# Kernel tuning notes

Hardware: AMD Instinct MI355X
Metric: run time of the kernel (lower is better)

## Reference

```python
import jax, jax.numpy as jnp
import numpy as np

N, E, F_IN, HID, NUM_CLASSES = 10000, 160000, 512, 1024, 100
NEG_SLOPE = 0.2  # PyG GATv2Conv default negative_slope


def setup_inputs() -> dict:
    key = jax.random.key(0)
    ks = jax.random.split(key, 10)
    return {
        "x": jax.random.normal(ks[0], (N, F_IN), jnp.float32),
        "edge_index": jax.random.randint(ks[1], (2, E), 0, N, dtype=jnp.int64)
        if jax.config.jax_enable_x64 else jax.random.randint(ks[1], (2, E), 0, N, dtype=jnp.int32),
        # GATv2Conv params (single head, out=1024): lin_l (source), lin_r (target), attention vector a, output bias
        "Wl": jax.random.normal(ks[2], (F_IN, HID), jnp.float32) / np.sqrt(F_IN),
        "bl": jnp.zeros((HID,), jnp.float32),
        "Wr": jax.random.normal(ks[3], (F_IN, HID), jnp.float32) / np.sqrt(F_IN),
        "br": jnp.zeros((HID,), jnp.float32),
        "att": jax.random.normal(ks[4], (HID,), jnp.float32) / np.sqrt(HID),
        "conv_b": jnp.zeros((HID,), jnp.float32),
        # MLP head: 1024 -> 512 -> 128 -> num_classes
        "W1": jax.random.normal(ks[5], (HID, 512), jnp.float32) / np.sqrt(HID),
        "b1": jnp.zeros((512,), jnp.float32),
        "W2": jax.random.normal(ks[6], (512, 128), jnp.float32) / np.sqrt(512),
        "b2": jnp.zeros((128,), jnp.float32),
        "Wc": jax.random.normal(ks[7], (128, NUM_CLASSES), jnp.float32) / np.sqrt(128),
        "bc": jnp.zeros((NUM_CLASSES,), jnp.float32),
    }


def _gatv2_conv(x, edge_index, Wl, bl, Wr, br, att, conv_b):
    """GATv2Conv, heads=1, add_self_loops=True, share_weights=False."""
    n = x.shape[0]
    loops = jnp.arange(n, dtype=edge_index.dtype)
    src = jnp.concatenate([edge_index[0], loops])  # message sources j
    dst = jnp.concatenate([edge_index[1], loops])  # message targets i
    xl = x @ Wl + bl  # [N, HID] source transform
    xr = x @ Wr + br  # [N, HID] target transform
    # e_ij = a^T LeakyReLU(xl_j + xr_i), per edge
    e = jax.nn.leaky_relu(xl[src] + xr[dst], negative_slope=NEG_SLOPE) @ att  # [E+N]
    # segment softmax over incoming edges of each target node (self-loops guarantee non-empty segments)
    m = jax.ops.segment_max(e, dst, num_segments=n)
    w = jnp.exp(e - m[dst])
    s = jax.ops.segment_sum(w, dst, num_segments=n)
    alpha = w / s[dst]  # [E+N]
    out = jax.ops.segment_sum(alpha[:, None] * xl[src], dst, num_segments=n)  # [N, HID]
    return out + conv_b


def reference(x, edge_index, Wl, bl, Wr, br, att, conv_b, W1, b1, W2, b2, Wc, bc):
    h = jax.nn.relu(_gatv2_conv(x, edge_index, Wl, bl, Wr, br, att, conv_b))
    h = jax.nn.relu(h @ W1 + b1)
    h = jax.nn.relu(h @ W2 + b2)
    return h @ Wc + bc
```

## Files before the change

kernel.cpp:

```cpp
#include <hip/hip_runtime.h>
#include <hip/hip_bf16.h>

constexpr int N_NODES = 10000;
constexpr int E_EDGES = 160000;
constexpr int F_IN    = 512;
constexpr int HID     = 1024;
constexpr int NCLS    = 100;
constexpr float NEG_SLOPE = 0.2f;

constexpr int BN = 128, BK = 32;
constexpr int M_PAD = 10112;
constexpr int DEG_CAP = 64;

typedef __attribute__((ext_vector_type(8))) short bf16x8;
typedef __attribute__((ext_vector_type(4))) float f32x4;
typedef __attribute__((ext_vector_type(2))) float f32x2;

__device__ inline void load_lds_16(const void* g, void* l) {
    __builtin_amdgcn_global_load_lds(
        (const __attribute__((address_space(1))) void*)g,
        (__attribute__((address_space(3))) void*)l, 16, 0, 0);
}

__device__ inline float rfl(float x) {
    return __builtin_bit_cast(float,
        __builtin_amdgcn_readfirstlane(__builtin_bit_cast(int, x)));
}

__device__ inline f32x2 bfpair(int d) {
    f32x2 r;
    r.x = __builtin_bit_cast(float, d << 16);
    r.y = __builtin_bit_cast(float, d & (int)0xffff0000);
    return r;
}

__device__ inline short4 cvt4(const f32x4 v, const float4 b, int relu) {
    float r0 = v[0] + b.x, r1 = v[1] + b.y, r2 = v[2] + b.z, r3 = v[3] + b.w;
    if (relu) {
        r0 = fmaxf(r0, 0.f); r1 = fmaxf(r1, 0.f);
        r2 = fmaxf(r2, 0.f); r3 = fmaxf(r3, 0.f);
    }
    short4 o;
    o.x = __builtin_bit_cast(short, __float2bfloat16(r0));
    o.y = __builtin_bit_cast(short, __float2bfloat16(r1));
    o.z = __builtin_bit_cast(short, __float2bfloat16(r2));
    o.w = __builtin_bit_cast(short, __float2bfloat16(r3));
    return o;
}

__global__ __launch_bounds__(256, 4) void gemm_mfma_64(
    const __hip_bfloat16* __restrict__ A, const __hip_bfloat16* __restrict__ Bt,
    const float* __restrict__ bias, int M, int K, int relu, int n_valid,
    __hip_bfloat16* __restrict__ Cb, int ldb)
{
    __shared__ __align__(16) short As[2][64 * BK];
    __shared__ __align__(16) short Bs[2][BN * BK];

    const int tid  = threadIdx.x;
    const int lane = tid & 63;
    const int w    = tid >> 6;
    const int m0   = blockIdx.y * 64;
    const int n0   = blockIdx.x * BN;

    f32x4 acc[4][2] = {};

    const int ca = tid;
    const int ra = ca >> 2, cca = (ca & 3) ^ ((ra >> 2) & 3);
    const int c0 = tid, c1 = tid + 256;
    const int r0 = c0 >> 2, cc0 = (c0 & 3) ^ ((r0 >> 2) & 3);
    const int r1 = c1 >> 2, cc1 = (c1 & 3) ^ ((r1 >> 2) & 3);

    const short* Ag  = (const short*)A + (size_t)(m0 + ra) * K + cca * 8;
    const short* Bg0 = (const short*)Bt + (size_t)(n0 + r0) * K + cc0 * 8;
    const short* Bg1 = (const short*)Bt + (size_t)(n0 + r1) * K + cc1 * 8;

    const int wn = w * 32;
    const int q  = lane >> 4;
    const int mr = lane & 15;
    const int sl = (q ^ (mr >> 2)) * 8;

    load_lds_16(Ag,  As[0] + ca * 8);
    load_lds_16(Bg0, Bs[0] + c0 * 8);
    load_lds_16(Bg1, Bs[0] + c1 * 8);

    int cur = 0;
    for (int k0 = 0; k0 < K; k0 += BK) {
        __syncthreads();
        const int nxt = cur ^ 1;
        const int kn = k0 + BK;
        if (kn < K) {
            load_lds_16(Ag + kn,  As[nxt] + ca * 8);
            load_lds_16(Bg0 + kn, Bs[nxt] + c0 * 8);
            load_lds_16(Bg1 + kn, Bs[nxt] + c1 * 8);
        }

        bf16x8 af[4], bf[2];
        #pragma unroll
        for (int mt = 0; mt < 4; ++mt)
            af[mt] = *(const bf16x8*)&As[cur][(mt * 16 + mr) * BK + sl];
        #pragma unroll
        for (int nt = 0; nt < 2; ++nt)
            bf[nt] = *(const bf16x8*)&Bs[cur][(wn + nt * 16 + mr) * BK + sl];
        #pragma unroll
        for (int mt = 0; mt < 4; ++mt)
            #pragma unroll
            for (int nt = 0; nt < 2; ++nt)
                acc[mt][nt] = __builtin_amdgcn_mfma_f32_16x16x32_bf16(
                    bf[nt], af[mt], acc[mt][nt], 0, 0, 0);
        cur = nxt;
    }

    #pragma unroll
    for (int mt = 0; mt < 4; ++mt) {
        const int gm = m0 + mt * 16 + mr;
        if (gm >= M) continue;
        #pragma unroll
        for (int nt = 0; nt < 2; ++nt) {
            const int gn = n0 + wn + nt * 16 + q * 4;
            if (gn >= n_valid) continue;
            const float4 bv = *(const float4*)&bias[gn];
            short4 o = cvt4(acc[mt][nt], bv, relu);
            *(short4*)((short*)Cb + (size_t)gm * ldb + gn) = o;
        }
    }
}

constexpr int HS_LD = 136;

__global__ __launch_bounds__(256) void mlp_tail(
    const __hip_bfloat16* __restrict__ h1, const __hip_bfloat16* __restrict__ W2t,
    const float* __restrict__ b2, const __hip_bfloat16* __restrict__ Wct,
    const float* __restrict__ bc, float* __restrict__ out)
{
    __shared__ __align__(16) short As[2][64 * BK];
    __shared__ __align__(16) short Bs[2][BN * BK];
    __shared__ __align__(16) short Hs[64 * HS_LD];

    const int tid  = threadIdx.x;
    const int lane = tid & 63;
    const int w    = tid >> 6;
    const int m0   = blockIdx.x * 64;

    const int ca = tid;
    const int ra = ca >> 2, cca = (ca & 3) ^ ((ra >> 2) & 3);
    const int c0 = tid, c1 = tid + 256;
    const int r0 = c0 >> 2, cc0 = (c0 & 3) ^ ((r0 >> 2) & 3);
    const int r1 = c1 >> 2, cc1 = (c1 & 3) ^ ((r1 >> 2) & 3);

    const int wn = w * 32;
    const int q  = lane >> 4;
    const int mr = lane & 15;
    const int sl = (q ^ (mr >> 2)) * 8;

    {
        f32x4 acc[4][2] = {};
        const short* Ag  = (const short*)h1 + (size_t)(m0 + ra) * 512 + cca * 8;
        const short* Bg0 = (const short*)W2t + (size_t)r0 * 512 + cc0 * 8;
        const short* Bg1 = (const short*)W2t + (size_t)r1 * 512 + cc1 * 8;

        load_lds_16(Ag,  As[0] + ca * 8);
        load_lds_16(Bg0, Bs[0] + c0 * 8);
        load_lds_16(Bg1, Bs[0] + c1 * 8);

        int cur = 0;
        for (int k0 = 0; k0 < 512; k0 += BK) {
            __syncthreads();
            const int nxt = cur ^ 1;
            const int kn = k0 + BK;
            if (kn < 512) {
                load_lds_16(Ag + kn,  As[nxt] + ca * 8);
                load_lds_16(Bg0 + kn, Bs[nxt] + c0 * 8);
                load_lds_16(Bg1 + kn, Bs[nxt] + c1 * 8);
            }
            bf16x8 af[4], bf[2];
            #pragma unroll
            for (int mt = 0; mt < 4; ++mt)
                af[mt] = *(const bf16x8*)&As[cur][(mt * 16 + mr) * BK + sl];
            #pragma unroll
            for (int nt = 0; nt < 2; ++nt)
                bf[nt] = *(const bf16x8*)&Bs[cur][(wn + nt * 16 + mr) * BK + sl];
            #pragma unroll
            for (int mt = 0; mt < 4; ++mt)
                #pragma unroll
                for (int nt = 0; nt < 2; ++nt)
                    acc[mt][nt] = __builtin_amdgcn_mfma_f32_16x16x32_bf16(
                        bf[nt], af[mt], acc[mt][nt], 0, 0, 0);
            cur = nxt;
        }
        __syncthreads();
        #pragma unroll
        for (int mt = 0; mt < 4; ++mt) {
            const int ml = mt * 16 + mr;
            #pragma unroll
            for (int nt = 0; nt < 2; ++nt) {
                const int nl = wn + nt * 16 + q * 4;
                const float4 bv = *(const float4*)&b2[nl];
                short4 o = cvt4(acc[mt][nt], bv, 1);
                *(short4*)&Hs[ml * HS_LD + nl] = o;
            }
        }
    }

    {
        f32x4 acc[4][2] = {};
        const short* Bg0 = (const short*)Wct + (size_t)r0 * 128 + cc0 * 8;
        const short* Bg1 = (const short*)Wct + (size_t)r1 * 128 + cc1 * 8;

        for (int k0 = 0; k0 < 128; k0 += BK) {
            __syncthreads();
            load_lds_16(Bg0 + k0, Bs[0] + c0 * 8);
            load_lds_16(Bg1 + k0, Bs[0] + c1 * 8);
            __syncthreads();

            bf16x8 af[4], bf[2];
            #pragma unroll
            for (int mt = 0; mt < 4; ++mt)
                af[mt] = *(const bf16x8*)&Hs[(mt * 16 + mr) * HS_LD + k0 + q * 8];
            #pragma unroll
            for (int nt = 0; nt < 2; ++nt)
                bf[nt] = *(const bf16x8*)&Bs[0][(wn + nt * 16 + mr) * BK + sl];
            #pragma unroll
            for (int mt = 0; mt < 4; ++mt)
                #pragma unroll
                for (int nt = 0; nt < 2; ++nt)
                    acc[mt][nt] = __builtin_amdgcn_mfma_f32_16x16x32_bf16(
                        bf[nt], af[mt], acc[mt][nt], 0, 0, 0);
        }
        #pragma unroll
        for (int mt = 0; mt < 4; ++mt) {
            const int gm = m0 + mt * 16 + mr;
            if (gm >= N_NODES) continue;
            #pragma unroll
            for (int nt = 0; nt < 2; ++nt) {
                const int gn = wn + nt * 16 + q * 4;
                if (gn >= NCLS) continue;
                const float4 bv = *(const float4*)&bc[gn];
                float4 o;
                o.x = acc[mt][nt][0] + bv.x;
                o.y = acc[mt][nt][1] + bv.y;
                o.z = acc[mt][nt][2] + bv.z;
                o.w = acc[mt][nt][3] + bv.w;
                *(float4*)(out + (size_t)gm * NCLS + gn) = o;
            }
        }
    }
}

__device__ void transpose_tile(const float* __restrict__ W,
                               __hip_bfloat16* __restrict__ Wt,
                               int K, int N, int NP, int bx, int by,
                               int tx, int ty, float (*t)[33])
{
    int n0 = bx * 32, k0 = by * 32;
    #pragma unroll
    for (int i = 0; i < 32; i += 8) {
        int k = k0 + ty + i, n = n0 + tx;
        t[ty + i][tx] = (k < K && n < N) ? W[(size_t)k * N + n] : 0.f;
    }
    __syncthreads();
    #pragma unroll
    for (int i = 0; i < 32; i += 8) {
        int n = n0 + ty + i, k = k0 + tx;
        if (n < NP && k < K)
            Wt[(size_t)n * K + k] = __float2bfloat16(t[tx][ty + i]);
    }
}

constexpr int PK_X    = M_PAD * F_IN / 1024;
constexpr int PK_WL   = PK_X + 512;
constexpr int PK_WR   = PK_WL + 512;
constexpr int PK_W1   = PK_WR + 512;
constexpr int PK_W2   = PK_W1 + 64;
constexpr int PK_WC   = PK_W2 + 16;
constexpr int PK_BLR  = PK_WC + 8;
constexpr int PK_EDGE = PK_BLR + (E_EDGES + N_NODES + 255) / 256;

__global__ __launch_bounds__(256) void pack_all(
    const float* __restrict__ x, __hip_bfloat16* __restrict__ xb,
    const float* __restrict__ Wl, const float* __restrict__ Wr,
    __hip_bfloat16* __restrict__ Wlrt,
    const float* __restrict__ W1, __hip_bfloat16* __restrict__ W1t,
    const float* __restrict__ W2, __hip_bfloat16* __restrict__ W2t,
    const float* __restrict__ Wc, __hip_bfloat16* __restrict__ Wct,
    const float* __restrict__ bl, const float* __restrict__ br,
    float* __restrict__ blr,
    const int* __restrict__ ei, int* __restrict__ cnt, int* __restrict__ srcs)
{
    __shared__ float t[32][33];
    const int b = blockIdx.x;
    const int tid = threadIdx.x;
    const int tx = tid & 31, ty = tid >> 5;

    if (b < PK_X) {
        int i = b * 256 + tid;
        int row = i >> 7;
        int base = i << 2;
        short4 o;
        if (row < N_NODES) {
            const float4 v = *(const float4*)(x + base);
            o.x = __builtin_bit_cast(short, __float2bfloat16(v.x));
            o.y = __builtin_bit_cast(short, __float2bfloat16(v.y));
            o.z = __builtin_bit_cast(short, __float2bfloat16(v.z));
            o.w = __builtin_bit_cast(short, __float2bfloat16(v.w));
        } else {
            o.x = o.y = o.z = o.w = 0;
        }
        *(short4*)((short*)xb + base) = o;
    } else if (b < PK_WL) {
        int l = b - PK_X;
        transpose_tile(Wl, Wlrt, F_IN, HID, HID, l & 31, l >> 5, tx, ty, t);
    } else if (b < PK_WR) {
        int l = b - PK_WL;
        transpose_tile(Wr, Wlrt + (size_t)HID * F_IN, F_IN, HID, HID,
                       l & 31, l >> 5, tx, ty, t);
    } else if (b < PK_W1) {
        int l = b - PK_WR;
        transpose_tile(W1, W1t, HID, 512, 512, l & 15, l >> 4, tx, ty, t);
    } else if (b < PK_W2) {
        int l = b - PK_W1;
        transpose_tile(W2, W2t, 512, 128, 128, l & 3, l >> 2, tx, ty, t);
    } else if (b < PK_WC) {
        int l = b - PK_W2;
        transpose_tile(Wc, Wct, 128, NCLS, 128, l & 3, l >> 2, tx, ty, t);
    } else if (b < PK_BLR) {
        int i = (b - PK_WC) * 256 + tid;
        if (i < HID) blr[i] = bl[i];
        else if (i < 2 * HID) blr[i] = br[i - HID];
    } else {
        int e = (b - PK_BLR) * 256 + tid;
        if (e < E_EDGES + N_NODES) {
            int s, d;
            if (e < E_EDGES) { s = ei[e]; d = ei[E_EDGES + e]; }
            else             { s = e - E_EDGES; d = s; }
            int r = atomicAdd(&cnt[d], 1);
            if (r < DEG_CAP) srcs[(size_t)d * DEG_CAP + r] = s;
        }
    }
}

__global__ __launch_bounds__(256) void gat_node(
    const __hip_bfloat16* __restrict__ xlr, const float* __restrict__ att,
    const float* __restrict__ conv_b,
    const int* __restrict__ cnt, const int* __restrict__ srcs,
    __hip_bfloat16* __restrict__ h)
{
    const int tid  = threadIdx.x;
    const int lane = tid & 63;
    const int wave = tid >> 6;
    const int nloc = wave >> 1;
    const int wsub = wave & 1;
    const int i    = blockIdx.x * 2 + nloc;

    __shared__ float O_s[2][16 * 64];
    __shared__ float ml_s[2][2];

    int deg = __builtin_amdgcn_readfirstlane(cnt[i]);
    if (deg > DEG_CAP) deg = DEG_CAP;
    const int last = deg - 1;
    const int* slist = srcs + (size_t)i * DEG_CAP;
    const short* base = (const short*)xlr;

    f32x2 xr2[8], att2[8];
    {
        const int4* xri = (const int4*)(base + (size_t)i * 2048 + HID + lane * 16);
        int4 a0 = xri[0], a1 = xri[1];
        xr2[0] = bfpair(a0.x); xr2[1] = bfpair(a0.y);
        xr2[2] = bfpair(a0.z); xr2[3] = bfpair(a0.w);
        xr2[4] = bfpair(a1.x); xr2[5] = bfpair(a1.y);
        xr2[6] = bfpair(a1.z); xr2[7] = bfpair(a1.w);
        const float* ai = att + lane * 16;
        #pragma unroll
        for (int k = 0; k < 8; ++k) {
            att2[k].x = ai[2 * k];
            att2[k].y = ai[2 * k + 1];
        }
    }

    float m_w = -3e38f, l_w = 0.f;
    f32x2 O2[8];
    #pragma unroll
    for (int k = 0; k < 8; ++k) O2[k] = f32x2{0.f, 0.f};

    int pos = wsub;
    if (pos < deg) {
        int sc = __builtin_amdgcn_readfirstlane(slist[pos]);
        if ((unsigned)sc >= N_NODES) sc = i;
        int sn = __builtin_amdgcn_readfirstlane(
                     slist[pos + 2 <= last ? pos + 2 : last]);
        if ((unsigned)sn >= N_NODES) sn = i;
        const int4* rp = (const int4*)(base + (size_t)sc * 2048 + lane * 16);
        int4 a0 = rp[0], a1 = rp[1];

        for (; pos < deg; pos += 2) {
            const int4* np = (const int4*)(base + (size_t)sn * 2048 + lane * 16);
            int4 b0 = np[0], b1 = np[1];
            int s2 = slist[pos + 4 <= last ? pos + 4 : last];

            f32x2 xf[8];
            xf[0] = bfpair(a0.x); xf[1] = bfpair(a0.y);
            xf[2] = bfpair(a0.z); xf[3] = bfpair(a0.w);
            xf[4] = bfpair(a1.x); xf[5] = bfpair(a1.y);
            xf[6] = bfpair(a1.z); xf[7] = bfpair(a1.w);

            f32x2 p2 = f32x2{0.f, 0.f};
            #pragma unroll
            for (int k = 0; k < 8; ++k) {
                f32x2 s = xf[k] + xr2[k];
                f32x2 t = s * NEG_SLOPE;
                s.x = fmaxf(s.x, t.x);
                s.y = fmaxf(s.y, t.y);
                p2 = __builtin_elementwise_fma(att2[k], s, p2);
            }
            float p = p2.x + p2.y;
            #pragma unroll
            for (int s = 1; s < 64; s <<= 1) p += __shfl_xor(p, s, 64);
            p = rfl(p);

            if (p > m_w) {
                const float scale = __expf(m_w - p);
                const f32x2 sc2 = f32x2{scale, scale};
                l_w = l_w * scale + 1.f;
                #pragma unroll
                for (int k = 0; k < 8; ++k)
                    O2[k] = __builtin_elementwise_fma(sc2, O2[k], xf[k]);
                m_w = p;
            } else {
                const float alpha = __expf(p - m_w);
                const f32x2 av = f32x2{alpha, alpha};
                l_w += alpha;
                #pragma unroll
                for (int k = 0; k < 8; ++k)
                    O2[k] = __builtin_elementwise_fma(av, xf[k], O2[k]);
            }

            a0 = b0; a1 = b1;
            sn = __builtin_amdgcn_readfirstlane(s2);
            if ((unsigned)sn >= N_NODES) sn = i;
        }
    }

    if (wsub == 1) {
        #pragma unroll
        for (int k = 0; k < 8; ++k) {
            O_s[nloc][(2 * k) * 64 + lane]     = O2[k].x;
            O_s[nloc][(2 * k + 1) * 64 + lane] = O2[k].y;
        }
        if (lane == 0) { ml_s[nloc][0] = m_w; ml_s[nloc][1] = l_w; }
    }
    __syncthreads();

    if (wsub == 0) {
        const float m1 = ml_s[nloc][0], l1 = ml_s[nloc][1];
        const float M  = fmaxf(m_w, m1);
        const float c0 = __expf(m_w - M);
        const float c1 = __expf(m1 - M);
        const float invL = 1.f / (l_w * c0 + l1 * c1);
        const float* cb = conv_b + lane * 16;
        bf16x8 o0, o1;
        #pragma unroll
        for (int k = 0; k < 8; ++k) {
            float ox = c0 * O2[k].x + c1 * O_s[nloc][(2 * k) * 64 + lane];
            float oy = c0 * O2[k].y + c1 * O_s[nloc][(2 * k + 1) * 64 + lane];
            float rx = fmaxf(__builtin_fmaf(ox, invL, cb[2 * k]), 0.f);
            float ry = fmaxf(__builtin_fmaf(oy, invL, cb[2 * k + 1]), 0.f);
            short sx = __builtin_bit_cast(short, __float2bfloat16(rx));
            short sy = __builtin_bit_cast(short, __float2bfloat16(ry));
            if (k < 4) { o0[2 * k] = sx; o0[2 * k + 1] = sy; }
            else       { o1[2 * (k - 4)] = sx; o1[2 * (k - 4) + 1] = sy; }
        }
        short* hp = (short*)h + (size_t)i * HID + lane * 16;
        *(bf16x8*)hp = o0;
        *(bf16x8*)(hp + 8) = o1;
    }
}

extern "C" void kernel_launch(void* const* d_in, const int* in_sizes, int n_in,
                              void* d_out, int out_size, void* d_ws, size_t ws_size,
                              hipStream_t stream)
{
    const float* x      = (const float*)d_in[0];
    const int*   ei     = (const int*)d_in[1];
    const float* Wl     = (const float*)d_in[2];
    const float* bl     = (const float*)d_in[3];
    const float* Wr     = (const float*)d_in[4];
    const float* br     = (const float*)d_in[5];
    const float* att    = (const float*)d_in[6];
    const float* conv_b = (const float*)d_in[7];
    const float* W1     = (const float*)d_in[8];
    const float* b1     = (const float*)d_in[9];
    const float* W2     = (const float*)d_in[10];
    const float* b2     = (const float*)d_in[11];
    const float* Wc     = (const float*)d_in[12];
    const float* bc     = (const float*)d_in[13];
    float* out = (float*)d_out;

    char* p = (char*)d_ws;
    __hip_bfloat16* xlr = (__hip_bfloat16*)p; p += (size_t)M_PAD * 2048 * 2;
    __hip_bfloat16* hb  = (__hip_bfloat16*)p; p += (size_t)M_PAD * HID * 2;
    __hip_bfloat16* xb  = (__hip_bfloat16*)p; p += (size_t)M_PAD * F_IN * 2;
    __hip_bfloat16* Wlrt= (__hip_bfloat16*)p; p += (size_t)2 * HID * F_IN * 2;
    __hip_bfloat16* W1t = (__hip_bfloat16*)p; p += (size_t)512 * HID * 2;
    __hip_bfloat16* W2t = (__hip_bfloat16*)p; p += (size_t)128 * 512 * 2;
    __hip_bfloat16* Wct = (__hip_bfloat16*)p; p += (size_t)128 * 128 * 2;
    float* blr = (float*)p;               p += 2 * HID * 4;
    int* cnt  = (int*)p;                  p += N_NODES * 4;
    int* srcs = (int*)p;                  p += (size_t)N_NODES * DEG_CAP * 4;

    __hip_bfloat16* h1 = xb;

    const dim3 blk(256);

    hipMemsetAsync(cnt, 0, N_NODES * sizeof(int), stream);

    pack_all<<<PK_EDGE, blk, 0, stream>>>(x, xb, Wl, Wr, Wlrt, W1, W1t,
                                          W2, W2t, Wc, Wct, bl, br, blr,
                                          ei, cnt, srcs);

    gemm_mfma_64<<<dim3(2 * HID / BN, M_PAD / 64), blk, 0, stream>>>(
        xb, Wlrt, blr, N_NODES, F_IN, 0, 2 * HID, xlr, 2048);

    gat_node<<<N_NODES / 2, blk, 0, stream>>>(xlr, att, conv_b, cnt, srcs, hb);

    gemm_mfma_64<<<dim3(512 / BN, M_PAD / 64), blk, 0, stream>>>(
        hb, W1t, b1, N_NODES, HID, 1, 512, h1, 512);

    mlp_tail<<<M_PAD / 64, blk, 0, stream>>>(h1, W2t, b2, Wct, bc, out);
}
```

Measured before the change: 236.7 us.

## Widen GEMM K-tile, preload classifier weights, unroll edge loop two-wide

The main GEMM now uses a 64-wide K tile with an 8-way XOR swizzle, halving loop iterations and barriers at the cost of twice the LDS and a lower occupancy hint. The MLP tail loads the whole classifier weight matrix into LDS up front, overlapping that load with the first GEMM and removing per-step barriers in the last layer. The GAT aggregation loop processes two edges per iteration with interleaved gathers and reductions, giving more memory-level parallelism at the cost of more registers.

```diff
diff --git a/kernel.cpp b/kernel.cpp
--- a/kernel.cpp
+++ b/kernel.cpp
@@ -8,7 +8,7 @@
 constexpr int NCLS    = 100;
 constexpr float NEG_SLOPE = 0.2f;
 
-constexpr int BN = 128, BK = 32;
+constexpr int BN = 128;
 constexpr int M_PAD = 10112;
 constexpr int DEG_CAP = 64;
 
@@ -48,11 +48,12 @@
     return o;
 }
 
-__global__ __launch_bounds__(256, 4) void gemm_mfma_64(
+__global__ __launch_bounds__(256, 3) void gemm_mfma_64(
     const __hip_bfloat16* __restrict__ A, const __hip_bfloat16* __restrict__ Bt,
     const float* __restrict__ bias, int M, int K, int relu, int n_valid,
     __hip_bfloat16* __restrict__ Cb, int ldb)
 {
+    constexpr int BK = 64;
     __shared__ __align__(16) short As[2][64 * BK];
     __shared__ __align__(16) short Bs[2][BN * BK];
 
@@ -64,24 +65,38 @@
 
     f32x4 acc[4][2] = {};
 
-    const int ca = tid;
-    const int ra = ca >> 2, cca = (ca & 3) ^ ((ra >> 2) & 3);
-    const int c0 = tid, c1 = tid + 256;
-    const int r0 = c0 >> 2, cc0 = (c0 & 3) ^ ((r0 >> 2) & 3);
-    const int r1 = c1 >> 2, cc1 = (c1 & 3) ^ ((r1 >> 2) & 3);
-
-    const short* Ag  = (const short*)A + (size_t)(m0 + ra) * K + cca * 8;
-    const short* Bg0 = (const short*)Bt + (size_t)(n0 + r0) * K + cc0 * 8;
-    const short* Bg1 = (const short*)Bt + (size_t)(n0 + r1) * K + cc1 * 8;
+    int ar[2], acs[2];
+    #pragma unroll
+    for (int j = 0; j < 2; ++j) {
+        int c = tid + 256 * j;
+        ar[j] = c >> 3;
+        acs[j] = ((c & 7) ^ (ar[j] & 7)) * 8;
+    }
+    int br_[4], bcs[4];
+    #pragma unroll
+    for (int j = 0; j < 4; ++j) {
+        int c = tid + 256 * j;
+        br_[j] = c >> 3;
+        bcs[j] = ((c & 7) ^ (br_[j] & 7)) * 8;
+    }
+
+    const short* Agp[2];
+    #pragma unroll
+    for (int j = 0; j < 2; ++j)
+        Agp[j] = (const short*)A + (size_t)(m0 + ar[j]) * K + acs[j];
+    const short* Bgp[4];
+    #pragma unroll
+    for (int j = 0; j < 4; ++j)
+        Bgp[j] = (const short*)Bt + (size_t)(n0 + br_[j]) * K + bcs[j];
 
     const int wn = w * 32;
     const int q  = lane >> 4;
     const int mr = lane & 15;
-    const int sl = (q ^ (mr >> 2)) * 8;
-
-    load_lds_16(Ag,  As[0] + ca * 8);
-    load_lds_16(Bg0, Bs[0] + c0 * 8);
-    load_lds_16(Bg1, Bs[0] + c1 * 8);
+
+    #pragma unroll
+    for (int j = 0; j < 2; ++j) load_lds_16(Agp[j], As[0] + (tid + 256 * j) * 8);
+    #pragma unroll
+    for (int j = 0; j < 4; ++j) load_lds_16(Bgp[j], Bs[0] + (tid + 256 * j) * 8);
 
     int cur = 0;
     for (int k0 = 0; k0 < K; k0 += BK) {
@@ -89,24 +104,31 @@
         const int nxt = cur ^ 1;
         const int kn = k0 + BK;
         if (kn < K) {
-            load_lds_16(Ag + kn,  As[nxt] + ca * 8);
-            load_lds_16(Bg0 + kn, Bs[nxt] + c0 * 8);
-            load_lds_16(Bg1 + kn, Bs[nxt] + c1 * 8);
-        }
-
-        bf16x8 af[4], bf[2];
-        #pragma unroll
-        for (int mt = 0; mt < 4; ++mt)
-            af[mt] = *(const bf16x8*)&As[cur][(mt * 16 + mr) * BK + sl];
-        #pragma unroll
-        for (int nt = 0; nt < 2; ++nt)
-            bf[nt] = *(const bf16x8*)&Bs[cur][(wn + nt * 16 + mr) * BK + sl];
-        #pragma unroll
-        for (int mt = 0; mt < 4; ++mt)
+            #pragma unroll
+            for (int j = 0; j < 2; ++j)
+                load_lds_16(Agp[j] + kn, As[nxt] + (tid + 256 * j) * 8);
+            #pragma unroll
+            for (int j = 0; j < 4; ++j)
+                load_lds_16(Bgp[j] + kn, Bs[nxt] + (tid + 256 * j) * 8);
+        }
+
+        #pragma unroll
+        for (int ks = 0; ks < 2; ++ks) {
+            const int sl = ((ks * 4 + q) ^ (mr & 7)) * 8;
+            bf16x8 af[4], bf[2];
+            #pragma unroll
+            for (int mt = 0; mt < 4; ++mt)
+                af[mt] = *(const bf16x8*)&As[cur][(mt * 16 + mr) * BK + sl];
             #pragma unroll
             for (int nt = 0; nt < 2; ++nt)
-                acc[mt][nt] = __builtin_amdgcn_mfma_f32_16x16x32_bf16(
-                    bf[nt], af[mt], acc[mt][nt], 0, 0, 0);
+                bf[nt] = *(const bf16x8*)&Bs[cur][(wn + nt * 16 + mr) * BK + sl];
+            #pragma unroll
+            for (int mt = 0; mt < 4; ++mt)
+                #pragma unroll
+                for (int nt = 0; nt < 2; ++nt)
+                    acc[mt][nt] = __builtin_amdgcn_mfma_f32_16x16x32_bf16(
+                        bf[nt], af[mt], acc[mt][nt], 0, 0, 0);
+        }
         cur = nxt;
     }
 
@@ -132,9 +154,11 @@
     const float* __restrict__ b2, const __hip_bfloat16* __restrict__ Wct,
     const float* __restrict__ bc, float* __restrict__ out)
 {
+    constexpr int BK = 32;
     __shared__ __align__(16) short As[2][64 * BK];
     __shared__ __align__(16) short Bs[2][BN * BK];
     __shared__ __align__(16) short Hs[64 * HS_LD];
+    __shared__ __align__(16) short Cs[128 * 128];
 
     const int tid  = threadIdx.x;
     const int lane = tid & 63;
@@ -151,6 +175,14 @@
     const int q  = lane >> 4;
     const int mr = lane & 15;
     const int sl = (q ^ (mr >> 2)) * 8;
+
+    #pragma unroll
+    for (int j = 0; j < 8; ++j) {
+        int c = tid + 256 * j;
+        int row = c >> 4;
+        int gcol = ((c & 15) ^ (row & 15)) * 8;
+        load_lds_16((const short*)Wct + (size_t)row * 128 + gcol, Cs + c * 8);
+    }
 
     {
         f32x4 acc[4][2] = {};
@@ -201,24 +233,22 @@
         }
     }
 
+    __syncthreads();
+
     {
         f32x4 acc[4][2] = {};
-        const short* Bg0 = (const short*)Wct + (size_t)r0 * 128 + cc0 * 8;
-        const short* Bg1 = (const short*)Wct + (size_t)r1 * 128 + cc1 * 8;
-
-        for (int k0 = 0; k0 < 128; k0 += BK) {
-            __syncthreads();
-            load_lds_16(Bg0 + k0, Bs[0] + c0 * 8);
-            load_lds_16(Bg1 + k0, Bs[0] + c1 * 8);
-            __syncthreads();
-
+        #pragma unroll
+        for (int kc = 0; kc < 4; ++kc) {
             bf16x8 af[4], bf[2];
             #pragma unroll
             for (int mt = 0; mt < 4; ++mt)
-                af[mt] = *(const bf16x8*)&Hs[(mt * 16 + mr) * HS_LD + k0 + q * 8];
-            #pragma unroll
-            for (int nt = 0; nt < 2; ++nt)
-                bf[nt] = *(const bf16x8*)&Bs[0][(wn + nt * 16 + mr) * BK + sl];
+                af[mt] = *(const bf16x8*)&Hs[(mt * 16 + mr) * HS_LD + kc * 32 + q * 8];
+            #pragma unroll
+            for (int nt = 0; nt < 2; ++nt) {
+                const int row = wn + nt * 16 + mr;
+                const int phys = ((kc * 4 + q) ^ (mr & 15)) * 8;
+                bf[nt] = *(const bf16x8*)&Cs[row * 128 + phys];
+            }
             #pragma unroll
             for (int mt = 0; mt < 4; ++mt)
                 #pragma unroll
@@ -356,7 +386,6 @@
 
     int deg = __builtin_amdgcn_readfirstlane(cnt[i]);
     if (deg > DEG_CAP) deg = DEG_CAP;
-    const int last = deg - 1;
     const int* slist = srcs + (size_t)i * DEG_CAP;
     const short* base = (const short*)xlr;
 
@@ -381,63 +410,108 @@
     #pragma unroll
     for (int k = 0; k < 8; ++k) O2[k] = f32x2{0.f, 0.f};
 
-    int pos = wsub;
-    if (pos < deg) {
-        int sc = __builtin_amdgcn_readfirstlane(slist[pos]);
-        if ((unsigned)sc >= N_NODES) sc = i;
-        int sn = __builtin_amdgcn_readfirstlane(
-                     slist[pos + 2 <= last ? pos + 2 : last]);
-        if ((unsigned)sn >= N_NODES) sn = i;
-        const int4* rp = (const int4*)(base + (size_t)sc * 2048 + lane * 16);
-        int4 a0 = rp[0], a1 = rp[1];
-
-        for (; pos < deg; pos += 2) {
-            const int4* np = (const int4*)(base + (size_t)sn * 2048 + lane * 16);
-            int4 b0 = np[0], b1 = np[1];
-            int s2 = slist[pos + 4 <= last ? pos + 4 : last];
-
-            f32x2 xf[8];
-            xf[0] = bfpair(a0.x); xf[1] = bfpair(a0.y);
-            xf[2] = bfpair(a0.z); xf[3] = bfpair(a0.w);
-            xf[4] = bfpair(a1.x); xf[5] = bfpair(a1.y);
-            xf[6] = bfpair(a1.z); xf[7] = bfpair(a1.w);
-
-            f32x2 p2 = f32x2{0.f, 0.f};
-            #pragma unroll
-            for (int k = 0; k < 8; ++k) {
-                f32x2 s = xf[k] + xr2[k];
-                f32x2 t = s * NEG_SLOPE;
-                s.x = fmaxf(s.x, t.x);
-                s.y = fmaxf(s.y, t.y);
-                p2 = __builtin_elementwise_fma(att2[k], s, p2);
+    const int nw = (deg - wsub + 1) >> 1;
+    const int lastt = nw - 1;
+
+#define EIDX(t) (wsub + 2 * ((t) < lastt ? (t) : lastt))
+#define GUARD(s) { if ((unsigned)(s) >= N_NODES) (s) = i; }
+#define CVT8(dst, v0, v1)                                                   \
+    dst[0] = bfpair(v0.x); dst[1] = bfpair(v0.y);                           \
+    dst[2] = bfpair(v0.z); dst[3] = bfpair(v0.w);                           \
+    dst[4] = bfpair(v1.x); dst[5] = bfpair(v1.y);                           \
+    dst[6] = bfpair(v1.z); dst[7] = bfpair(v1.w);
+#define DOT(p2, xf)                                                         \
+    {                                                                       \
+        p2 = f32x2{0.f, 0.f};                                               \
+        _Pragma("unroll")                                                   \
+        for (int k = 0; k < 8; ++k) {                                       \
+            f32x2 s = xf[k] + xr2[k];                                       \
+            f32x2 u = s * NEG_SLOPE;                                        \
+            s.x = fmaxf(s.x, u.x);                                          \
+            s.y = fmaxf(s.y, u.y);                                          \
+            p2 = __builtin_elementwise_fma(att2[k], s, p2);                 \
+        }                                                                   \
+    }
+#define UPDATE(p, xf)                                                       \
+    {                                                                       \
+        if ((p) > m_w) {                                                    \
+            const float scale = __expf(m_w - (p));                          \
+            const f32x2 sc2 = f32x2{scale, scale};                          \
+            l_w = l_w * scale + 1.f;                                        \
+            _Pragma("unroll")                                               \
+            for (int k = 0; k < 8; ++k)                                     \
+                O2[k] = __builtin_elementwise_fma(sc2, O2[k], xf[k]);       \
+            m_w = (p);                                                      \
+        } else {                                                            \
+            const float alpha = __expf((p)-m_w);                            \
+            const f32x2 av = f32x2{alpha, alpha};                           \
+            l_w += alpha;                                                   \
+            _Pragma("unroll")                                               \
+            for (int k = 0; k < 8; ++k)                                     \
+                O2[k] = __builtin_elementwise_fma(av, xf[k], O2[k]);        \
+        }                                                                   \
+    }
+
+    if (nw > 0) {
+        int sA = __builtin_amdgcn_readfirstlane(slist[EIDX(0)]); GUARD(sA);
+        int sC = __builtin_amdgcn_readfirstlane(slist[EIDX(1)]); GUARD(sC);
+        const int4* ap = (const int4*)(base + (size_t)sA * 2048 + lane * 16);
+        const int4* cp = (const int4*)(base + (size_t)sC * 2048 + lane * 16);
+        int4 A0 = ap[0], A1 = ap[1];
+        int4 C0 = cp[0], C1 = cp[1];
+        int pA = slist[EIDX(2)];
+        int pC = slist[EIDX(3)];
+
+        int t = 0;
+        for (; t + 1 < nw; t += 2) {
+            int snA = __builtin_amdgcn_readfirstlane(pA); GUARD(snA);
+            int snC = __builtin_amdgcn_readfirstlane(pC); GUARD(snC);
+            const int4* bp = (const int4*)(base + (size_t)snA * 2048 + lane * 16);
+            const int4* dp = (const int4*)(base + (size_t)snC * 2048 + lane * 16);
+            int4 B0 = bp[0], B1 = bp[1];
+            int4 D0 = dp[0], D1 = dp[1];
+            pA = slist[EIDX(t + 4)];
+            pC = slist[EIDX(t + 5)];
+
+            f32x2 xfA[8], xfC[8];
+            CVT8(xfA, A0, A1);
+            CVT8(xfC, C0, C1);
+
+            f32x2 p2a, p2c;
+            DOT(p2a, xfA);
+            DOT(p2c, xfC);
+            float pa = p2a.x + p2a.y;
+            float pc = p2c.x + p2c.y;
+            #pragma unroll
+            for (int s = 1; s < 64; s <<= 1) {
+                pa += __shfl_xor(pa, s, 64);
+                pc += __shfl_xor(pc, s, 64);
             }
-            float p = p2.x + p2.y;
-            #pragma unroll
-            for (int s = 1; s < 64; s <<= 1) p += __shfl_xor(p, s, 64);
-            p = rfl(p);
-
-            if (p > m_w) {
-                const float scale = __expf(m_w - p);
-                const f32x2 sc2 = f32x2{scale, scale};
-                l_w = l_w * scale + 1.f;
-                #pragma unroll
-                for (int k = 0; k < 8; ++k)
-                    O2[k] = __builtin_elementwise_fma(sc2, O2[k], xf[k]);
-                m_w = p;
-            } else {
-                const float alpha = __expf(p - m_w);
-                const f32x2 av = f32x2{alpha, alpha};
-                l_w += alpha;
-                #pragma unroll
-                for (int k = 0; k < 8; ++k)
-                    O2[k] = __builtin_elementwise_fma(av, xf[k], O2[k]);
-            }
-
-            a0 = b0; a1 = b1;
-            sn = __builtin_amdgcn_readfirstlane(s2);
-            if ((unsigned)sn >= N_NODES) sn = i;
-        }
-    }
+            pa = rfl(pa);
+            pc = rfl(pc);
+
+            UPDATE(pa, xfA);
+            UPDATE(pc, xfC);
+
+            A0 = B0; A1 = B1; C0 = D0; C1 = D1;
+        }
+        if (t < nw) {
+            f32x2 xfA[8];
+            CVT8(xfA, A0, A1);
+            f32x2 p2a;
+            DOT(p2a, xfA);
+            float pa = p2a.x + p2a.y;
+            #pragma unroll
+            for (int s = 1; s < 64; s <<= 1) pa += __shfl_xor(pa, s, 64);
+            pa = rfl(pa);
+            UPDATE(pa, xfA);
+        }
+    }
+#undef EIDX
+#undef GUARD
+#undef CVT8
+#undef DOT
+#undef UPDATE
 
     if (wsub == 1) {
         #pragma unroll
```

Result: no change. 232.5 us (-1.8%).

## Split GAT nodes over four waves, deepen GEMM K-tile, preload classifier weights

Applied to the files above, without the earlier changes.

The GAT aggregation kernel now gives each node a whole 256-thread block, so four waves split the incoming edges instead of two. Their partial online-softmax states are merged through shared memory. The main GEMM moves from a K tile of 32 to 64 with an 8-way XOR swizzle and launch bounds lowered to 3 waves per SIMD, halving the number of loop barriers per tile. The MLP tail loads the whole 128x128 classifier weight into LDS once, which removes per-step barriers but costs extra LDS and may lower occupancy.

```diff
diff --git a/kernel.cpp b/kernel.cpp
--- a/kernel.cpp
+++ b/kernel.cpp
@@ -8,7 +8,7 @@
 constexpr int NCLS    = 100;
 constexpr float NEG_SLOPE = 0.2f;
 
-constexpr int BN = 128, BK = 32;
+constexpr int BN = 128;
 constexpr int M_PAD = 10112;
 constexpr int DEG_CAP = 64;
 
@@ -48,11 +48,12 @@
     return o;
 }
 
-__global__ __launch_bounds__(256, 4) void gemm_mfma_64(
+__global__ __launch_bounds__(256, 3) void gemm_mfma_64(
     const __hip_bfloat16* __restrict__ A, const __hip_bfloat16* __restrict__ Bt,
     const float* __restrict__ bias, int M, int K, int relu, int n_valid,
     __hip_bfloat16* __restrict__ Cb, int ldb)
 {
+    constexpr int BK = 64;
     __shared__ __align__(16) short As[2][64 * BK];
     __shared__ __align__(16) short Bs[2][BN * BK];
 
@@ -64,24 +65,38 @@
 
     f32x4 acc[4][2] = {};
 
-    const int ca = tid;
-    const int ra = ca >> 2, cca = (ca & 3) ^ ((ra >> 2) & 3);
-    const int c0 = tid, c1 = tid + 256;
-    const int r0 = c0 >> 2, cc0 = (c0 & 3) ^ ((r0 >> 2) & 3);
-    const int r1 = c1 >> 2, cc1 = (c1 & 3) ^ ((r1 >> 2) & 3);
-
-    const short* Ag  = (const short*)A + (size_t)(m0 + ra) * K + cca * 8;
-    const short* Bg0 = (const short*)Bt + (size_t)(n0 + r0) * K + cc0 * 8;
-    const short* Bg1 = (const short*)Bt + (size_t)(n0 + r1) * K + cc1 * 8;
+    int ar[2], acs[2];
+    #pragma unroll
+    for (int j = 0; j < 2; ++j) {
+        int c = tid + 256 * j;
+        ar[j] = c >> 3;
+        acs[j] = ((c & 7) ^ (ar[j] & 7)) * 8;
+    }
+    int br_[4], bcs[4];
+    #pragma unroll
+    for (int j = 0; j < 4; ++j) {
+        int c = tid + 256 * j;
+        br_[j] = c >> 3;
+        bcs[j] = ((c & 7) ^ (br_[j] & 7)) * 8;
+    }
+
+    const short* Agp[2];
+    #pragma unroll
+    for (int j = 0; j < 2; ++j)
+        Agp[j] = (const short*)A + (size_t)(m0 + ar[j]) * K + acs[j];
+    const short* Bgp[4];
+    #pragma unroll
+    for (int j = 0; j < 4; ++j)
+        Bgp[j] = (const short*)Bt + (size_t)(n0 + br_[j]) * K + bcs[j];
 
     const int wn = w * 32;
     const int q  = lane >> 4;
     const int mr = lane & 15;
-    const int sl = (q ^ (mr >> 2)) * 8;
-
-    load_lds_16(Ag,  As[0] + ca * 8);
-    load_lds_16(Bg0, Bs[0] + c0 * 8);
-    load_lds_16(Bg1, Bs[0] + c1 * 8);
+
+    #pragma unroll
+    for (int j = 0; j < 2; ++j) load_lds_16(Agp[j], As[0] + (tid + 256 * j) * 8);
+    #pragma unroll
+    for (int j = 0; j < 4; ++j) load_lds_16(Bgp[j], Bs[0] + (tid + 256 * j) * 8);
 
     int cur = 0;
     for (int k0 = 0; k0 < K; k0 += BK) {
@@ -89,24 +104,31 @@
         const int nxt = cur ^ 1;
         const int kn = k0 + BK;
         if (kn < K) {
-            load_lds_16(Ag + kn,  As[nxt] + ca * 8);
-            load_lds_16(Bg0 + kn, Bs[nxt] + c0 * 8);
-            load_lds_16(Bg1 + kn, Bs[nxt] + c1 * 8);
-        }
-
-        bf16x8 af[4], bf[2];
-        #pragma unroll
-        for (int mt = 0; mt < 4; ++mt)
-            af[mt] = *(const bf16x8*)&As[cur][(mt * 16 + mr) * BK + sl];
-        #pragma unroll
-        for (int nt = 0; nt < 2; ++nt)
-            bf[nt] = *(const bf16x8*)&Bs[cur][(wn + nt * 16 + mr) * BK + sl];
-        #pragma unroll
-        for (int mt = 0; mt < 4; ++mt)
+            #pragma unroll
+            for (int j = 0; j < 2; ++j)
+                load_lds_16(Agp[j] + kn, As[nxt] + (tid + 256 * j) * 8);
+            #pragma unroll
+            for (int j = 0; j < 4; ++j)
+                load_lds_16(Bgp[j] + kn, Bs[nxt] + (tid + 256 * j) * 8);
+        }
+
+        #pragma unroll
+        for (int ks = 0; ks < 2; ++ks) {
+            const int sl = ((ks * 4 + q) ^ (mr & 7)) * 8;
+            bf16x8 af[4], bf[2];
+            #pragma unroll
+            for (int mt = 0; mt < 4; ++mt)
+                af[mt] = *(const bf16x8*)&As[cur][(mt * 16 + mr) * BK + sl];
             #pragma unroll
             for (int nt = 0; nt < 2; ++nt)
-                acc[mt][nt] = __builtin_amdgcn_mfma_f32_16x16x32_bf16(
-                    bf[nt], af[mt], acc[mt][nt], 0, 0, 0);
+                bf[nt] = *(const bf16x8*)&Bs[cur][(wn + nt * 16 + mr) * BK + sl];
+            #pragma unroll
+            for (int mt = 0; mt < 4; ++mt)
+                #pragma unroll
+                for (int nt = 0; nt < 2; ++nt)
+                    acc[mt][nt] = __builtin_amdgcn_mfma_f32_16x16x32_bf16(
+                        bf[nt], af[mt], acc[mt][nt], 0, 0, 0);
+        }
         cur = nxt;
     }
 
@@ -132,9 +154,11 @@
     const float* __restrict__ b2, const __hip_bfloat16* __restrict__ Wct,
     const float* __restrict__ bc, float* __restrict__ out)
 {
+    constexpr int BK = 32;
     __shared__ __align__(16) short As[2][64 * BK];
     __shared__ __align__(16) short Bs[2][BN * BK];
     __shared__ __align__(16) short Hs[64 * HS_LD];
+    __shared__ __align__(16) short Cs[128 * 128];
 
     const int tid  = threadIdx.x;
     const int lane = tid & 63;
@@ -151,6 +175,14 @@
     const int q  = lane >> 4;
     const int mr = lane & 15;
     const int sl = (q ^ (mr >> 2)) * 8;
+
+    #pragma unroll
+    for (int j = 0; j < 8; ++j) {
+        int c = tid + 256 * j;
+        int row = c >> 4;
+        int gcol = ((c & 15) ^ (row & 15)) * 8;
+        load_lds_16((const short*)Wct + (size_t)row * 128 + gcol, Cs + c * 8);
+    }
 
     {
         f32x4 acc[4][2] = {};
@@ -201,24 +233,22 @@
         }
     }
 
+    __syncthreads();
+
     {
         f32x4 acc[4][2] = {};
-        const short* Bg0 = (const short*)Wct + (size_t)r0 * 128 + cc0 * 8;
-        const short* Bg1 = (const short*)Wct + (size_t)r1 * 128 + cc1 * 8;
-
-        for (int k0 = 0; k0 < 128; k0 += BK) {
-            __syncthreads();
-            load_lds_16(Bg0 + k0, Bs[0] + c0 * 8);
-            load_lds_16(Bg1 + k0, Bs[0] + c1 * 8);
-            __syncthreads();
-
+        #pragma unroll
+        for (int kc = 0; kc < 4; ++kc) {
             bf16x8 af[4], bf[2];
             #pragma unroll
             for (int mt = 0; mt < 4; ++mt)
-                af[mt] = *(const bf16x8*)&Hs[(mt * 16 + mr) * HS_LD + k0 + q * 8];
-            #pragma unroll
-            for (int nt = 0; nt < 2; ++nt)
-                bf[nt] = *(const bf16x8*)&Bs[0][(wn + nt * 16 + mr) * BK + sl];
+                af[mt] = *(const bf16x8*)&Hs[(mt * 16 + mr) * HS_LD + kc * 32 + q * 8];
+            #pragma unroll
+            for (int nt = 0; nt < 2; ++nt) {
+                const int row = wn + nt * 16 + mr;
+                const int phys = ((kc * 4 + q) ^ (mr & 15)) * 8;
+                bf[nt] = *(const bf16x8*)&Cs[row * 128 + phys];
+            }
             #pragma unroll
             for (int mt = 0; mt < 4; ++mt)
                 #pragma unroll
@@ -347,12 +377,10 @@
     const int tid  = threadIdx.x;
     const int lane = tid & 63;
     const int wave = tid >> 6;
-    const int nloc = wave >> 1;
-    const int wsub = wave & 1;
-    const int i    = blockIdx.x * 2 + nloc;
-
-    __shared__ float O_s[2][16 * 64];
-    __shared__ float ml_s[2][2];
+    const int i    = blockIdx.x;
+
+    __shared__ float O_s[3][16 * 64];
+    __shared__ float ml_s[3][2];
 
     int deg = __builtin_amdgcn_readfirstlane(cnt[i]);
     if (deg > DEG_CAP) deg = DEG_CAP;
@@ -381,20 +409,21 @@
     #pragma unroll
     for (int k = 0; k < 8; ++k) O2[k] = f32x2{0.f, 0.f};
 
-    int pos = wsub;
+    int pos = wave;
     if (pos < deg) {
         int sc = __builtin_amdgcn_readfirstlane(slist[pos]);
         if ((unsigned)sc >= N_NODES) sc = i;
-        int sn = __builtin_amdgcn_readfirstlane(
-                     slist[pos + 2 <= last ? pos + 2 : last]);
+        int pn = (pos + 4 <= last) ? pos + 4 : last;
+        int sn = __builtin_amdgcn_readfirstlane(slist[pn]);
         if ((unsigned)sn >= N_NODES) sn = i;
         const int4* rp = (const int4*)(base + (size_t)sc * 2048 + lane * 16);
         int4 a0 = rp[0], a1 = rp[1];
 
-        for (; pos < deg; pos += 2) {
+        for (; pos < deg; pos += 4) {
             const int4* np = (const int4*)(base + (size_t)sn * 2048 + lane * 16);
             int4 b0 = np[0], b1 = np[1];
-            int s2 = slist[pos + 4 <= last ? pos + 4 : last];
+            int p2i = (pos + 8 <= last) ? pos + 8 : last;
+            int s2 = slist[p2i];
 
             f32x2 xf[8];
             xf[0] = bfpair(a0.x); xf[1] = bfpair(a0.y);
@@ -406,9 +435,9 @@
             #pragma unroll
             for (int k = 0; k < 8; ++k) {
                 f32x2 s = xf[k] + xr2[k];
-                f32x2 t = s * NEG_SLOPE;
-                s.x = fmaxf(s.x, t.x);
-                s.y = fmaxf(s.y, t.y);
+                f32x2 u = s * NEG_SLOPE;
+                s.x = fmaxf(s.x, u.x);
+                s.y = fmaxf(s.y, u.y);
                 p2 = __builtin_elementwise_fma(att2[k], s, p2);
             }
             float p = p2.x + p2.y;
@@ -439,28 +468,40 @@
         }
     }
 
-    if (wsub == 1) {
+    if (wave > 0) {
         #pragma unroll
         for (int k = 0; k < 8; ++k) {
-            O_s[nloc][(2 * k) * 64 + lane]     = O2[k].x;
-            O_s[nloc][(2 * k + 1) * 64 + lane] = O2[k].y;
-        }
-        if (lane == 0) { ml_s[nloc][0] = m_w; ml_s[nloc][1] = l_w; }
+            O_s[wave - 1][(2 * k) * 64 + lane]     = O2[k].x;
+            O_s[wave - 1][(2 * k + 1) * 64 + lane] = O2[k].y;
+        }
+        if (lane == 0) { ml_s[wave - 1][0] = m_w; ml_s[wave - 1][1] = l_w; }
     }
     __syncthreads();
 
-    if (wsub == 0) {
-        const float m1 = ml_s[nloc][0], l1 = ml_s[nloc][1];
-        const float M  = fmaxf(m_w, m1);
+    if (wave == 0) {
+        float M = m_w;
+        #pragma unroll
+        for (int w2 = 0; w2 < 3; ++w2) M = fmaxf(M, ml_s[w2][0]);
         const float c0 = __expf(m_w - M);
-        const float c1 = __expf(m1 - M);
-        const float invL = 1.f / (l_w * c0 + l1 * c1);
+        float cs[3];
+        float L = l_w * c0;
+        #pragma unroll
+        for (int w2 = 0; w2 < 3; ++w2) {
+            cs[w2] = __expf(ml_s[w2][0] - M);
+            L += ml_s[w2][1] * cs[w2];
+        }
+        const float invL = 1.f / L;
         const float* cb = conv_b + lane * 16;
         bf16x8 o0, o1;
         #pragma unroll
         for (int k = 0; k < 8; ++k) {
-            float ox = c0 * O2[k].x + c1 * O_s[nloc][(2 * k) * 64 + lane];
-            float oy = c0 * O2[k].y + c1 * O_s[nloc][(2 * k + 1) * 64 + lane];
+            float ox = c0 * O2[k].x;
+            float oy = c0 * O2[k].y;
+            #pragma unroll
+            for (int w2 = 0; w2 < 3; ++w2) {
+                ox += cs[w2] * O_s[w2][(2 * k) * 64 + lane];
+                oy += cs[w2] * O_s[w2][(2 * k + 1) * 64 + lane];
+            }
             float rx = fmaxf(__builtin_fmaf(ox, invL, cb[2 * k]), 0.f);
             float ry = fmaxf(__builtin_fmaf(oy, invL, cb[2 * k + 1]), 0.f);
             short sx = __builtin_bit_cast(short, __float2bfloat16(rx));
@@ -519,7 +560,7 @@
     gemm_mfma_64<<<dim3(2 * HID / BN, M_PAD / 64), blk, 0, stream>>>(
         xb, Wlrt, blr, N_NODES, F_IN, 0, 2 * HID, xlr, 2048);
 
-    gat_node<<<N_NODES / 2, blk, 0, stream>>>(xlr, att, conv_b, cnt, srcs, hb);
+    gat_node<<<N_NODES, blk, 0, stream>>>(xlr, att, conv_b, cnt, srcs, hb);
 
     gemm_mfma_64<<<dim3(512 / BN, M_PAD / 64), blk, 0, stream>>>(
         hb, W1t, b1, N_NODES, HID, 1, 512, h1, 512);
```

Result: no change. 233.2 us (-1.5%).
